# Kernel tuning notes

Hardware: AMD Instinct MI355X
Metric: run time of the kernel (lower is better)

Reference implementation:

```python
import jax, jax.numpy as jnp
import numpy as np

B, H, S, D = 2, 16, 2048, 64

def setup_inputs() -> dict:
    key = jax.random.key(0)
    kq, kk, kv = jax.random.split(key, 3)
    query = jax.random.normal(kq, (B, H, S, D), dtype=jnp.float32)
    key_t = jax.random.normal(kk, (B, H, S, D), dtype=jnp.float32)
    value = jax.random.normal(kv, (B, H, S, D), dtype=jnp.float32)
    return {"query": query, "key": key_t, "value": value}

def reference(query, key, value):
    d_k = query.shape[-1]
    scale = 1.0 / jnp.sqrt(jnp.asarray(d_k, dtype=query.dtype))
    # scores: [B, H, S, S]
    scores = jnp.einsum('bhqd,bhkd->bhqk', query, key) * scale
    p_attn = jax.nn.softmax(scores, axis=-1)
    output = jnp.einsum('bhqk,bhkd->bhqd', p_attn, value)
    return (output, p_attn)
```

## Files before the change

kernel.cpp:

```cpp
#include <hip/hip_runtime.h>

#define SS 2048
#define DD 64
#define QB 64
#define KVB 64
#define NT (SS / KVB)

typedef unsigned short ushort_t;
typedef __attribute__((ext_vector_type(4)))  float f32x4;
typedef __attribute__((ext_vector_type(16))) float f32x16;
typedef __attribute__((ext_vector_type(8)))  short bf16x8;
typedef __attribute__((ext_vector_type(2)))  unsigned int u32x2;

static __device__ __forceinline__ unsigned short f2bf(float f) {
    unsigned u = __builtin_bit_cast(unsigned, f);
    u += 0x7FFFu + ((u >> 16) & 1u);
    return (unsigned short)(u >> 16);
}

static __device__ __forceinline__ f32x16 zero16() {
    f32x16 z;
#pragma unroll
    for (int i = 0; i < 16; ++i) z[i] = 0.f;
    return z;
}

union PFrag { bf16x8 v; unsigned w[4]; };

#define GLL16(src, dst) \
    __builtin_amdgcn_global_load_lds((const __attribute__((address_space(1))) void*)(src), \
                                     (__attribute__((address_space(3))) void*)(dst), 16, 0, 0)

__global__ void cvt_bf16(const float* __restrict__ src, ushort_t* __restrict__ dst,
                         int n8, float scale)
{
    int i = blockIdx.x * blockDim.x + threadIdx.x;
    if (i >= n8) return;
    f32x4 a = ((const f32x4*)src)[2 * i];
    f32x4 b = ((const f32x4*)src)[2 * i + 1];
    bf16x8 o;
#pragma unroll
    for (int j = 0; j < 4; ++j) o[j] = (short)f2bf(a[j] * scale);
#pragma unroll
    for (int j = 0; j < 4; ++j) o[4 + j] = (short)f2bf(b[j] * scale);
    ((bf16x8*)dst)[i] = o;
}

__global__ void transposeV(const float* __restrict__ V, ushort_t* __restrict__ Vt)
{
    __shared__ float tile[64][65];
    const int tid = threadIdx.x;
    const int hh = blockIdx.x >> 5;
    const int kt = blockIdx.x & 31;

#pragma unroll
    for (int it = 0; it < 4; ++it) {
        int m = it * 256 + tid;
        int r = m >> 4, c4 = m & 15;
        f32x4 v = *(const f32x4*)(V + ((size_t)(hh * SS + kt * 64 + r)) * DD + c4 * 4);
#pragma unroll
        for (int j = 0; j < 4; ++j) tile[r][c4 * 4 + j] = v[j];
    }
    __syncthreads();
#pragma unroll
    for (int it = 0; it < 2; ++it) {
        int m = it * 256 + tid;
        int d = m >> 3, c8 = m & 7;
        bf16x8 o;
#pragma unroll
        for (int j = 0; j < 8; ++j) o[j] = (short)f2bf(tile[c8 * 8 + j][d]);
        *(bf16x8*)(Vt + ((size_t)hh * DD + d) * SS + kt * 64 + c8 * 8) = o;
    }
}

__global__ __launch_bounds__(256, 4)
void attn_main4(const float* __restrict__ gQ, const ushort_t* __restrict__ Kbf,
                const ushort_t* __restrict__ Vtbf, float* __restrict__ gO,
                float* __restrict__ gP)
{
    __shared__ float lsm[4][32];
    __shared__ __attribute__((aligned(16))) char shraw[33792];
    ushort_t* stage = (ushort_t*)shraw;
    float*    osm   = (float*)shraw;

    const int tid  = threadIdx.x;
    const int lane = tid & 63;
    const int wave = tid >> 6;
    const int lo5  = lane & 31;
    const int hi   = lane >> 5;
    const int qs   = wave >> 1;
    const int sub  = wave & 1;

    const int bid  = blockIdx.x;
    const int wg   = (bid & 7) * 128 + (bid >> 3);
    const int head = wg >> 5;
    const int q0b  = (wg & 31) * QB;

    const float*    Qh = gQ   + (size_t)head * SS * DD;
    const ushort_t* Kh = Kbf  + (size_t)head * SS * DD;
    const ushort_t* Vh = Vtbf + (size_t)head * DD * SS;
    float* Oh = gO + (size_t)head * SS * DD;
    float* Ph = gP + (size_t)head * SS * SS;

    const float SCALE = 0.125f * 1.44269504088896340736f;

    const int qrow = q0b + qs * 32 + lo5;
    bf16x8 qf[4];
#pragma unroll
    for (int ks = 0; ks < 4; ++ks) {
        const float* qp = Qh + (size_t)qrow * DD + ks * 16 + hi * 8;
        f32x4 a = *(const f32x4*)(qp);
        f32x4 b = *(const f32x4*)(qp + 4);
        bf16x8 o;
#pragma unroll
        for (int j = 0; j < 4; ++j) o[j] = (short)f2bf(a[j] * SCALE);
#pragma unroll
        for (int j = 0; j < 4; ++j) o[4 + j] = (short)f2bf(b[j] * SCALE);
        qf[ks] = o;
    }

    const int lgrp = lane >> 3;
    const int lchk = (lane & 7) ^ lgrp;
    const ushort_t* srcK[2]; const ushort_t* srcV[2];
#pragma unroll
    for (int j = 0; j < 2; ++j) {
        int W = wave * 2 + j;
        srcK[j] = Kh + (size_t)(W * 8 + lgrp) * DD + lchk * 8;
        srcV[j] = Vh + (size_t)(W * 8 + lgrp) * SS + lchk * 8;
    }
    const int kvl = sub * 32 + lo5;

#pragma unroll
    for (int j = 0; j < 2; ++j) GLL16(srcK[j], stage + (wave * 2 + j) * 512);
    __syncthreads();

    float ls0 = 0.f, ls1 = 0.f;
    for (int t = 0; t < NT; ++t) {
        const int buf = t & 1;
        if (t + 1 < NT) {
#pragma unroll
            for (int j = 0; j < 2; ++j)
                GLL16(srcK[j] + (size_t)(t + 1) * KVB * DD,
                      stage + (buf ^ 1) * 8192 + (wave * 2 + j) * 512);
        }
        const ushort_t* Ksb = stage + buf * 8192;
        f32x16 acc = zero16();
#pragma unroll
        for (int ks = 0; ks < 4; ++ks) {
            bf16x8 kf = *(const bf16x8*)(Ksb + kvl * 64 + ((((ks * 2) + hi) ^ (kvl & 7)) << 3));
            acc = __builtin_amdgcn_mfma_f32_32x32x16_bf16(kf, qf[ks], acc, 0, 0, 0);
        }
#pragma unroll
        for (int r = 0; r < 16; r += 2) {
            ls0 += __builtin_exp2f(acc[r]);
            ls1 += __builtin_exp2f(acc[r + 1]);
        }
        __syncthreads();
    }
    float lsum = ls0 + ls1;
    lsum += __shfl_xor(lsum, 32);
    lsm[wave][lo5] = lsum;
    __syncthreads();
    const float rinv = 1.0f / (lsm[qs * 2][lo5] + lsm[qs * 2 + 1][lo5]);

    f32x16 o0 = zero16(), o1 = zero16();
    float* prow_base = Ph + (size_t)qrow * SS;

#pragma unroll
    for (int j = 0; j < 2; ++j) {
        GLL16(srcK[j], stage + (wave * 2 + j) * 512);
        GLL16(srcV[j], stage + 4096 + (wave * 2 + j) * 512);
    }
    __syncthreads();

    for (int t = 0; t < NT; ++t) {
        const int buf = t & 1;
        if (t + 1 < NT) {
#pragma unroll
            for (int j = 0; j < 2; ++j) {
                GLL16(srcK[j] + (size_t)(t + 1) * KVB * DD,
                      stage + (buf ^ 1) * 8192 + (wave * 2 + j) * 512);
                GLL16(srcV[j] + (size_t)(t + 1) * KVB,
                      stage + (buf ^ 1) * 8192 + 4096 + (wave * 2 + j) * 512);
            }
        }
        const ushort_t* Ksb = stage + buf * 8192;
        const ushort_t* Vtb = Ksb + 4096;

        f32x16 acc = zero16();
#pragma unroll
        for (int ks = 0; ks < 4; ++ks) {
            bf16x8 kf = *(const bf16x8*)(Ksb + kvl * 64 + ((((ks * 2) + hi) ^ (kvl & 7)) << 3));
            acc = __builtin_amdgcn_mfma_f32_32x32x16_bf16(kf, qf[ks], acc, 0, 0, 0);
        }
        float pr[16];
#pragma unroll
        for (int r = 0; r < 16; ++r) pr[r] = __builtin_exp2f(acc[r]);

        float* prow = prow_base + t * KVB + sub * 32;
#pragma unroll
        for (int g = 0; g < 4; ++g) {
            f32x4 st = { pr[4*g+0] * rinv, pr[4*g+1] * rinv, pr[4*g+2] * rinv, pr[4*g+3] * rinv };
            *(f32x4*)(prow + g * 8 + hi * 4) = st;
        }

        unsigned u[8];
#pragma unroll
        for (int j = 0; j < 8; ++j)
            u[j] = (unsigned)f2bf(pr[2*j]) | ((unsigned)f2bf(pr[2*j+1]) << 16);

        unsigned s0 = __shfl_xor(u[0], 32), s1 = __shfl_xor(u[1], 32);
        unsigned s2 = __shfl_xor(u[2], 32), s3 = __shfl_xor(u[3], 32);
        unsigned s4 = __shfl_xor(u[4], 32), s5 = __shfl_xor(u[5], 32);
        unsigned s6 = __shfl_xor(u[6], 32), s7 = __shfl_xor(u[7], 32);
        PFrag pf0, pf1;
        pf0.w[0] = hi ? s2 : u[0];  pf0.w[1] = hi ? s3 : u[1];
        pf0.w[2] = hi ? u[2] : s0;  pf0.w[3] = hi ? u[3] : s1;
        pf1.w[0] = hi ? s6 : u[4];  pf1.w[1] = hi ? s7 : u[5];
        pf1.w[2] = hi ? u[6] : s4;  pf1.w[3] = hi ? u[7] : s5;

#pragma unroll
        for (int dt = 0; dt < 2; ++dt) {
            int drow = dt * 32 + lo5;
            int c0 = ((sub * 4) + 0 + hi) ^ (drow & 7);
            int c1 = ((sub * 4) + 2 + hi) ^ (drow & 7);
            bf16x8 vf0 = *(const bf16x8*)(Vtb + drow * 64 + (c0 << 3));
            bf16x8 vf1 = *(const bf16x8*)(Vtb + drow * 64 + (c1 << 3));
            f32x16& od = dt ? o1 : o0;
            od = __builtin_amdgcn_mfma_f32_32x32x16_bf16(vf0, pf0.v, od, 0, 0, 0);
            od = __builtin_amdgcn_mfma_f32_32x32x16_bf16(vf1, pf1.v, od, 0, 0, 0);
        }

        __syncthreads();
    }

#pragma unroll
    for (int dt = 0; dt < 2; ++dt) {
        const f32x16& od = dt ? o1 : o0;
#pragma unroll
        for (int g = 0; g < 4; ++g) {
#pragma unroll
            for (int j = 0; j < 4; ++j) {
                int d = dt * 32 + g * 8 + hi * 4 + j;
                osm[(wave * 64 + d) * 33 + lo5] = od[4 * g + j];
            }
        }
    }
    __syncthreads();
    {
        const int p  = tid >> 7;
        const int q  = (tid >> 2) & 31;
        const int d0 = (tid & 3) * 16;
        const float rq = 1.0f / (lsm[2 * p][q] + lsm[2 * p + 1][q]);
        float* op = Oh + (size_t)(q0b + p * 32 + q) * DD + d0;
#pragma unroll
        for (int v4 = 0; v4 < 4; ++v4) {
            f32x4 st;
#pragma unroll
            for (int j = 0; j < 4; ++j) {
                int d = d0 + v4 * 4 + j;
                st[j] = (osm[((2 * p) * 64 + d) * 33 + q] +
                         osm[((2 * p + 1) * 64 + d) * 33 + q]) * rq;
            }
            *(f32x4*)(op + v4 * 4) = st;
        }
    }
}

__global__ __launch_bounds__(256, 2)
void attn_fused(const float* __restrict__ gQ, const float* __restrict__ gK,
                const float* __restrict__ gV, float* __restrict__ gO,
                float* __restrict__ gP)
{
    __shared__ unsigned short Qs[128 * DD];
    __shared__ unsigned short Ks[64 * DD];
    __shared__ unsigned short Vt[DD * 64];

    const int tid  = threadIdx.x;
    const int lane = tid & 63;
    const int wave = tid >> 6;
    const int lo5  = lane & 31;
    const int hi   = lane >> 5;

    const int head = blockIdx.x >> 4;
    const int q0b  = (blockIdx.x & 15) * 128;

    const float* Qh = gQ + (size_t)head * SS * DD;
    const float* Kh = gK + (size_t)head * SS * DD;
    const float* Vh = gV + (size_t)head * SS * DD;
    float* Oh = gO + (size_t)head * SS * DD;
    float* Ph = gP + (size_t)head * SS * SS;

    const float SCALE = 0.125f * 1.44269504088896340736f;

#pragma unroll
    for (int it = 0; it < 8; ++it) {
        int m = it * 256 + tid;
        int q = m >> 4, d4 = m & 15;
        f32x4 v = *(const f32x4*)(Qh + (size_t)(q0b + q) * DD + d4 * 4);
        unsigned a = (unsigned)f2bf(v.x * SCALE) | ((unsigned)f2bf(v.y * SCALE) << 16);
        unsigned b = (unsigned)f2bf(v.z * SCALE) | ((unsigned)f2bf(v.w * SCALE) << 16);
        u32x2 w; w.x = a; w.y = b;
        *(u32x2*)(Qs + q * 64 + d4 * 4) = w;
    }
    __syncthreads();

    const int qrow = wave * 32 + lo5;
    bf16x8 qf[4];
#pragma unroll
    for (int ks = 0; ks < 4; ++ks)
        qf[ks] = *(const bf16x8*)(Qs + qrow * 64 + ks * 16 + hi * 8);

    auto stageK = [&](int kv0) {
#pragma unroll
        for (int it = 0; it < 4; ++it) {
            int m = it * 256 + tid;
            int kv = m >> 4, d4 = m & 15;
            f32x4 v = *(const f32x4*)(Kh + (size_t)(kv0 + kv) * DD + d4 * 4);
            unsigned a = (unsigned)f2bf(v.x) | ((unsigned)f2bf(v.y) << 16);
            unsigned b = (unsigned)f2bf(v.z) | ((unsigned)f2bf(v.w) << 16);
            int c16 = (d4 >> 1) ^ (kv & 7);
            u32x2 w; w.x = a; w.y = b;
            *(u32x2*)(Ks + kv * 64 + c16 * 8 + (d4 & 1) * 4) = w;
        }
    };
    auto stageV = [&](int kv0) {
#pragma unroll
        for (int it = 0; it < 2; ++it) {
            int m = it * 256 + tid;
            int kv2 = m >> 4, d4 = m & 15;
            const float* p0 = Vh + (size_t)(kv0 + kv2 * 2) * DD + d4 * 4;
            f32x4 v0 = *(const f32x4*)(p0);
            f32x4 v1 = *(const f32x4*)(p0 + DD);
#pragma unroll
            for (int c = 0; c < 4; ++c) {
                int d = d4 * 4 + c;
                unsigned u = (unsigned)f2bf(v0[c]) | ((unsigned)f2bf(v1[c]) << 16);
                int c16 = (kv2 >> 2) ^ (d & 7);
                *(unsigned*)(Vt + d * 64 + c16 * 8 + (kv2 & 3) * 2) = u;
            }
        }
    };

    float m_run = -1e30f, l_run = 0.f;
    for (int kv0 = 0; kv0 < SS; kv0 += 64) {
        __syncthreads();
        stageK(kv0);
        __syncthreads();
#pragma unroll
        for (int sub = 0; sub < 2; ++sub) {
            f32x16 acc = zero16();
            int kvl = sub * 32 + lo5;
#pragma unroll
            for (int ks = 0; ks < 4; ++ks) {
                bf16x8 kf = *(const bf16x8*)(Ks + kvl * 64 + ((((ks * 2) + hi) ^ (kvl & 7)) << 3));
                acc = __builtin_amdgcn_mfma_f32_32x32x16_bf16(kf, qf[ks], acc, 0, 0, 0);
            }
            float tm = acc[0];
#pragma unroll
            for (int r = 1; r < 16; ++r) tm = fmaxf(tm, acc[r]);
            float mn = fmaxf(m_run, tm);
            float sum = 0.f;
#pragma unroll
            for (int r = 0; r < 16; ++r) sum += __builtin_exp2f(acc[r] - mn);
            l_run = l_run * __builtin_exp2f(m_run - mn) + sum;
            m_run = mn;
        }
    }
    {
        float mo = __shfl_xor(m_run, 32);
        float mf = fmaxf(m_run, mo);
        float la = l_run * __builtin_exp2f(m_run - mf);
        float lb = __shfl_xor(la, 32);
        l_run = la + lb;
        m_run = mf;
    }
    const float rinv = 1.0f / l_run;

    f32x16 o0 = zero16(), o1 = zero16();
    const int qg = q0b + wave * 32 + lo5;
    float* prow_base = Ph + (size_t)qg * SS;

    for (int kv0 = 0; kv0 < SS; kv0 += 64) {
        __syncthreads();
        stageK(kv0);
        stageV(kv0);
        __syncthreads();
#pragma unroll
        for (int sub = 0; sub < 2; ++sub) {
            f32x16 acc = zero16();
            int kvl = sub * 32 + lo5;
#pragma unroll
            for (int ks = 0; ks < 4; ++ks) {
                bf16x8 kf = *(const bf16x8*)(Ks + kvl * 64 + ((((ks * 2) + hi) ^ (kvl & 7)) << 3));
                acc = __builtin_amdgcn_mfma_f32_32x32x16_bf16(kf, qf[ks], acc, 0, 0, 0);
            }
            float pr[16];
#pragma unroll
            for (int r = 0; r < 16; ++r) pr[r] = __builtin_exp2f(acc[r] - m_run);

            float* prow = prow_base + kv0 + sub * 32;
#pragma unroll
            for (int g = 0; g < 4; ++g) {
                f32x4 st = { pr[4*g+0] * rinv, pr[4*g+1] * rinv, pr[4*g+2] * rinv, pr[4*g+3] * rinv };
                *(f32x4*)(prow + g * 8 + hi * 4) = st;
            }

            unsigned u[8];
#pragma unroll
            for (int j = 0; j < 8; ++j)
                u[j] = (unsigned)f2bf(pr[2*j]) | ((unsigned)f2bf(pr[2*j+1]) << 16);

            unsigned s0 = __shfl_xor(u[0], 32), s1 = __shfl_xor(u[1], 32);
            unsigned s2 = __shfl_xor(u[2], 32), s3 = __shfl_xor(u[3], 32);
            unsigned s4 = __shfl_xor(u[4], 32), s5 = __shfl_xor(u[5], 32);
            unsigned s6 = __shfl_xor(u[6], 32), s7 = __shfl_xor(u[7], 32);
            PFrag pf0, pf1;
            pf0.w[0] = hi ? s2 : u[0];  pf0.w[1] = hi ? s3 : u[1];
            pf0.w[2] = hi ? u[2] : s0;  pf0.w[3] = hi ? u[3] : s1;
            pf1.w[0] = hi ? s6 : u[4];  pf1.w[1] = hi ? s7 : u[5];
            pf1.w[2] = hi ? u[6] : s4;  pf1.w[3] = hi ? u[7] : s5;

#pragma unroll
            for (int dt = 0; dt < 2; ++dt) {
                int drow = dt * 32 + lo5;
                int c0 = ((sub * 4) + 0 + hi) ^ (drow & 7);
                int c1 = ((sub * 4) + 2 + hi) ^ (drow & 7);
                bf16x8 vf0 = *(const bf16x8*)(Vt + drow * 64 + (c0 << 3));
                bf16x8 vf1 = *(const bf16x8*)(Vt + drow * 64 + (c1 << 3));
                f32x16& od = dt ? o1 : o0;
                od = __builtin_amdgcn_mfma_f32_32x32x16_bf16(vf0, pf0.v, od, 0, 0, 0);
                od = __builtin_amdgcn_mfma_f32_32x32x16_bf16(vf1, pf1.v, od, 0, 0, 0);
            }
        }
    }

    float* orow = Oh + (size_t)qg * DD;
#pragma unroll
    for (int dt = 0; dt < 2; ++dt) {
        const f32x16& od = dt ? o1 : o0;
#pragma unroll
        for (int g = 0; g < 4; ++g) {
            f32x4 st = { od[4*g+0] * rinv, od[4*g+1] * rinv, od[4*g+2] * rinv, od[4*g+3] * rinv };
            *(f32x4*)(orow + dt * 32 + g * 8 + hi * 4) = st;
        }
    }
}

extern "C" void kernel_launch(void* const* d_in, const int* in_sizes, int n_in,
                              void* d_out, int out_size, void* d_ws, size_t ws_size,
                              hipStream_t stream) {
    const float* Q = (const float*)d_in[0];
    const float* K = (const float*)d_in[1];
    const float* V = (const float*)d_in[2];
    float* O = (float*)d_out;
    float* P = O + (size_t)2 * 16 * SS * DD;

    const size_t HD = (size_t)32 * SS * DD;
    const size_t need = 2 * HD * sizeof(ushort_t);

    if (ws_size >= need) {
        ushort_t* Kbf  = (ushort_t*)d_ws;
        ushort_t* Vtbf = Kbf + HD;
        int n8 = (int)(HD / 8);
        hipLaunchKernelGGL(cvt_bf16, dim3(n8 / 256), dim3(256), 0, stream, K, Kbf, n8, 1.0f);
        hipLaunchKernelGGL(transposeV, dim3(1024), dim3(256), 0, stream, V, Vtbf);
        hipLaunchKernelGGL(attn_main4, dim3(1024), dim3(256), 0, stream, Q, Kbf, Vtbf, O, P);
    } else {
        hipLaunchKernelGGL(attn_fused, dim3(512), dim3(256), 0, stream, Q, K, V, O, P);
    }
}
```

Baseline: 212.3 us.

## Split row-sum pass into separate kernel with finer work split

Moves the softmax denominator computation out of the main attention kernel into a separate l_pass kernel. That kernel uses 32-row query blocks and splits the KV range across four waves, reading K directly from global memory with no LDS staging or barriers. The reciprocal row sums go to workspace and are read by b_pass, which now only computes P and O. This aims for more parallelism and less synchronization in the first pass, at the cost of an extra launch, a larger workspace requirement, and K being read again from global memory.

```diff
diff --git a/kernel.cpp b/kernel.cpp
--- a/kernel.cpp
+++ b/kernel.cpp
@@ -74,11 +74,78 @@
 }
 
 __global__ __launch_bounds__(256, 4)
-void attn_main4(const float* __restrict__ gQ, const ushort_t* __restrict__ Kbf,
-                const ushort_t* __restrict__ Vtbf, float* __restrict__ gO,
-                float* __restrict__ gP)
+void l_pass(const float* __restrict__ gQ, const ushort_t* __restrict__ Kbf,
+            float* __restrict__ wsR)
 {
     __shared__ float lsm[4][32];
+
+    const int tid  = threadIdx.x;
+    const int lane = tid & 63;
+    const int wave = tid >> 6;
+    const int lo5  = lane & 31;
+    const int hi   = lane >> 5;
+
+    const int bid  = blockIdx.x;
+    const int wg   = (bid & 7) * 256 + (bid >> 3);
+    const int head = wg >> 6;
+    const int q0b  = (wg & 63) * 32;
+
+    const float*    Qh = gQ  + (size_t)head * SS * DD;
+    const ushort_t* Kh = Kbf + (size_t)head * SS * DD;
+
+    const float SCALE = 0.125f * 1.44269504088896340736f;
+
+    const int qrow = q0b + lo5;
+    bf16x8 qf[4];
+#pragma unroll
+    for (int ks = 0; ks < 4; ++ks) {
+        const float* qp = Qh + (size_t)qrow * DD + ks * 16 + hi * 8;
+        f32x4 a = *(const f32x4*)(qp);
+        f32x4 b = *(const f32x4*)(qp + 4);
+        bf16x8 o;
+#pragma unroll
+        for (int j = 0; j < 4; ++j) o[j] = (short)f2bf(a[j] * SCALE);
+#pragma unroll
+        for (int j = 0; j < 4; ++j) o[4 + j] = (short)f2bf(b[j] * SCALE);
+        qf[ks] = o;
+    }
+
+    const int kv_base = wave * 512;
+    float ls0 = 0.f, ls1 = 0.f;
+#pragma unroll 2
+    for (int t = 0; t < 8; ++t) {
+        int kv0 = kv_base + t * 64;
+#pragma unroll
+        for (int sub = 0; sub < 2; ++sub) {
+            f32x16 acc = zero16();
+            const ushort_t* kp = Kh + (size_t)(kv0 + sub * 32 + lo5) * DD + hi * 8;
+#pragma unroll
+            for (int ks = 0; ks < 4; ++ks) {
+                bf16x8 kf = *(const bf16x8*)(kp + ks * 16);
+                acc = __builtin_amdgcn_mfma_f32_32x32x16_bf16(kf, qf[ks], acc, 0, 0, 0);
+            }
+#pragma unroll
+            for (int r = 0; r < 16; r += 2) {
+                ls0 += __builtin_exp2f(acc[r]);
+                ls1 += __builtin_exp2f(acc[r + 1]);
+            }
+        }
+    }
+    float lsum = ls0 + ls1;
+    lsum += __shfl_xor(lsum, 32);
+    lsm[wave][lo5] = lsum;
+    __syncthreads();
+    if (tid < 32) {
+        float l = lsm[0][tid] + lsm[1][tid] + lsm[2][tid] + lsm[3][tid];
+        wsR[(size_t)head * SS + q0b + tid] = 1.0f / l;
+    }
+}
+
+__global__ __launch_bounds__(256, 4)
+void b_pass(const float* __restrict__ gQ, const ushort_t* __restrict__ Kbf,
+            const ushort_t* __restrict__ Vtbf, const float* __restrict__ wsR,
+            float* __restrict__ gO, float* __restrict__ gP)
+{
     __shared__ __attribute__((aligned(16))) char shraw[33792];
     ushort_t* stage = (ushort_t*)shraw;
     float*    osm   = (float*)shraw;
@@ -118,6 +185,7 @@
         for (int j = 0; j < 4; ++j) o[4 + j] = (short)f2bf(b[j] * SCALE);
         qf[ks] = o;
     }
+    const float rinv = wsR[(size_t)head * SS + qrow];
 
     const int lgrp = lane >> 3;
     const int lchk = (lane & 7) ^ lgrp;
@@ -129,39 +197,6 @@
         srcV[j] = Vh + (size_t)(W * 8 + lgrp) * SS + lchk * 8;
     }
     const int kvl = sub * 32 + lo5;
-
-#pragma unroll
-    for (int j = 0; j < 2; ++j) GLL16(srcK[j], stage + (wave * 2 + j) * 512);
-    __syncthreads();
-
-    float ls0 = 0.f, ls1 = 0.f;
-    for (int t = 0; t < NT; ++t) {
-        const int buf = t & 1;
-        if (t + 1 < NT) {
-#pragma unroll
-            for (int j = 0; j < 2; ++j)
-                GLL16(srcK[j] + (size_t)(t + 1) * KVB * DD,
-                      stage + (buf ^ 1) * 8192 + (wave * 2 + j) * 512);
-        }
-        const ushort_t* Ksb = stage + buf * 8192;
-        f32x16 acc = zero16();
-#pragma unroll
-        for (int ks = 0; ks < 4; ++ks) {
-            bf16x8 kf = *(const bf16x8*)(Ksb + kvl * 64 + ((((ks * 2) + hi) ^ (kvl & 7)) << 3));
-            acc = __builtin_amdgcn_mfma_f32_32x32x16_bf16(kf, qf[ks], acc, 0, 0, 0);
-        }
-#pragma unroll
-        for (int r = 0; r < 16; r += 2) {
-            ls0 += __builtin_exp2f(acc[r]);
-            ls1 += __builtin_exp2f(acc[r + 1]);
-        }
-        __syncthreads();
-    }
-    float lsum = ls0 + ls1;
-    lsum += __shfl_xor(lsum, 32);
-    lsm[wave][lo5] = lsum;
-    __syncthreads();
-    const float rinv = 1.0f / (lsm[qs * 2][lo5] + lsm[qs * 2 + 1][lo5]);
 
     f32x16 o0 = zero16(), o1 = zero16();
     float* prow_base = Ph + (size_t)qrow * SS;
@@ -251,7 +286,7 @@
         const int p  = tid >> 7;
         const int q  = (tid >> 2) & 31;
         const int d0 = (tid & 3) * 16;
-        const float rq = 1.0f / (lsm[2 * p][q] + lsm[2 * p + 1][q]);
+        const float rq = wsR[(size_t)head * SS + q0b + p * 32 + q];
         float* op = Oh + (size_t)(q0b + p * 32 + q) * DD + d0;
 #pragma unroll
         for (int v4 = 0; v4 < 4; ++v4) {
@@ -457,15 +492,18 @@
     float* P = O + (size_t)2 * 16 * SS * DD;
 
     const size_t HD = (size_t)32 * SS * DD;
-    const size_t need = 2 * HD * sizeof(ushort_t);
+    const size_t RN = (size_t)32 * SS;
+    const size_t need = 2 * HD * sizeof(ushort_t) + RN * sizeof(float);
 
     if (ws_size >= need) {
         ushort_t* Kbf  = (ushort_t*)d_ws;
         ushort_t* Vtbf = Kbf + HD;
+        float*    wsR  = (float*)(Vtbf + HD);
         int n8 = (int)(HD / 8);
         hipLaunchKernelGGL(cvt_bf16, dim3(n8 / 256), dim3(256), 0, stream, K, Kbf, n8, 1.0f);
         hipLaunchKernelGGL(transposeV, dim3(1024), dim3(256), 0, stream, V, Vtbf);
-        hipLaunchKernelGGL(attn_main4, dim3(1024), dim3(256), 0, stream, Q, Kbf, Vtbf, O, P);
+        hipLaunchKernelGGL(l_pass, dim3(2048), dim3(256), 0, stream, Q, Kbf, wsR);
+        hipLaunchKernelGGL(b_pass, dim3(1024), dim3(256), 0, stream, Q, Kbf, Vtbf, wsR, O, P);
     } else {
         hipLaunchKernelGGL(attn_fused, dim3(512), dim3(256), 0, stream, Q, K, V, O, P);
     }
```

Result: slower. 256.3 us (+20.7%).

## Split row-sum pass across waves and use per-wave private K/V staging

Applied to the files above, without the earlier changes.

In the first pass (softmax denominators), each wave now reads its own quarter of the keys straight from global memory for both 32-row query halves. The per-wave sums are then combined through shared memory, which removes the per-tile block barriers from that pass. In the second pass, each wave double-buffers its own K/V slice in a private 16 KB LDS region, waits with explicit vmcnt counts, and skips the per-iteration __syncthreads. The cost is twice the LDS (64 KB) and a cut in occupancy from 4 to 2 blocks. It also adds redundant K loads across waves and hand-tuned waitcnt logic that could break if the compiler reorders loads.

```diff
diff --git a/kernel.cpp b/kernel.cpp
--- a/kernel.cpp
+++ b/kernel.cpp
@@ -73,13 +73,13 @@
     }
 }
 
-__global__ __launch_bounds__(256, 4)
-void attn_main4(const float* __restrict__ gQ, const ushort_t* __restrict__ Kbf,
+__global__ __launch_bounds__(256, 2)
+void attn_main7(const float* __restrict__ gQ, const ushort_t* __restrict__ Kbf,
                 const ushort_t* __restrict__ Vtbf, float* __restrict__ gO,
                 float* __restrict__ gP)
 {
-    __shared__ float lsm[4][32];
-    __shared__ __attribute__((aligned(16))) char shraw[33792];
+    __shared__ float lsm[4][2][32];
+    __shared__ __attribute__((aligned(16))) char shraw[65536];
     ushort_t* stage = (ushort_t*)shraw;
     float*    osm   = (float*)shraw;
 
@@ -104,94 +104,105 @@
 
     const float SCALE = 0.125f * 1.44269504088896340736f;
 
+    bf16x8 qf2[2][4];
+#pragma unroll
+    for (int p = 0; p < 2; ++p)
+#pragma unroll
+        for (int ks = 0; ks < 4; ++ks) {
+            const float* qp = Qh + (size_t)(q0b + p * 32 + lo5) * DD + ks * 16 + hi * 8;
+            f32x4 a = *(const f32x4*)(qp);
+            f32x4 b = *(const f32x4*)(qp + 4);
+            bf16x8 o;
+#pragma unroll
+            for (int j = 0; j < 4; ++j) o[j] = (short)f2bf(a[j] * SCALE);
+#pragma unroll
+            for (int j = 0; j < 4; ++j) o[4 + j] = (short)f2bf(b[j] * SCALE);
+            qf2[p][ks] = o;
+        }
+
+    float la00 = 0.f, la01 = 0.f, la10 = 0.f, la11 = 0.f;
+#pragma unroll 2
+    for (int t = 0; t < 8; ++t) {
+        int kv0 = wave * 512 + t * 64;
+#pragma unroll
+        for (int s = 0; s < 2; ++s) {
+            const ushort_t* kp = Kh + (size_t)(kv0 + s * 32 + lo5) * DD + hi * 8;
+            bf16x8 kf[4];
+#pragma unroll
+            for (int ks = 0; ks < 4; ++ks) kf[ks] = *(const bf16x8*)(kp + ks * 16);
+            f32x16 a0 = zero16(), a1 = zero16();
+#pragma unroll
+            for (int ks = 0; ks < 4; ++ks) {
+                a0 = __builtin_amdgcn_mfma_f32_32x32x16_bf16(kf[ks], qf2[0][ks], a0, 0, 0, 0);
+                a1 = __builtin_amdgcn_mfma_f32_32x32x16_bf16(kf[ks], qf2[1][ks], a1, 0, 0, 0);
+            }
+#pragma unroll
+            for (int r = 0; r < 16; r += 2) {
+                la00 += __builtin_exp2f(a0[r]);
+                la01 += __builtin_exp2f(a0[r + 1]);
+                la10 += __builtin_exp2f(a1[r]);
+                la11 += __builtin_exp2f(a1[r + 1]);
+            }
+        }
+    }
+    {
+        float l0 = la00 + la01, l1 = la10 + la11;
+        l0 += __shfl_xor(l0, 32);
+        l1 += __shfl_xor(l1, 32);
+        lsm[wave][0][lo5] = l0;
+        lsm[wave][1][lo5] = l1;
+    }
+    __syncthreads();
+    const float rinv = 1.0f / (lsm[0][qs][lo5] + lsm[1][qs][lo5] +
+                               lsm[2][qs][lo5] + lsm[3][qs][lo5]);
+
+    ushort_t* wbase = stage + wave * 8192;
+
+    const int l8g = lane >> 3, l8c = lane & 7;
+    const int kchk = l8c ^ l8g;
+    const int l4g = lane >> 2, l4c = lane & 3;
+    const int vchk = l4c ^ (l4g & 3);
+    const ushort_t* sK[4];
+    const ushort_t* sV[4];
+#pragma unroll
+    for (int j = 0; j < 4; ++j) {
+        sK[j] = Kh + (size_t)(sub * 32 + j * 8 + l8g) * DD + kchk * 8;
+        sV[j] = Vh + (size_t)(j * 16 + l4g) * SS + sub * 32 + vchk * 8;
+    }
+
+    auto STAGE_B = [&](int tt, int b) {
+        ushort_t* kb = wbase + b * 4096;
+#pragma unroll
+        for (int j = 0; j < 4; ++j)
+            GLL16(sK[j] + (size_t)tt * KVB * DD, kb + j * 512);
+#pragma unroll
+        for (int j = 0; j < 4; ++j)
+            GLL16(sV[j] + tt * KVB, kb + 2048 + j * 512);
+    };
+
+    f32x16 o0 = zero16(), o1 = zero16();
     const int qrow = q0b + qs * 32 + lo5;
-    bf16x8 qf[4];
-#pragma unroll
-    for (int ks = 0; ks < 4; ++ks) {
-        const float* qp = Qh + (size_t)qrow * DD + ks * 16 + hi * 8;
-        f32x4 a = *(const f32x4*)(qp);
-        f32x4 b = *(const f32x4*)(qp + 4);
-        bf16x8 o;
-#pragma unroll
-        for (int j = 0; j < 4; ++j) o[j] = (short)f2bf(a[j] * SCALE);
-#pragma unroll
-        for (int j = 0; j < 4; ++j) o[4 + j] = (short)f2bf(b[j] * SCALE);
-        qf[ks] = o;
-    }
-
-    const int lgrp = lane >> 3;
-    const int lchk = (lane & 7) ^ lgrp;
-    const ushort_t* srcK[2]; const ushort_t* srcV[2];
-#pragma unroll
-    for (int j = 0; j < 2; ++j) {
-        int W = wave * 2 + j;
-        srcK[j] = Kh + (size_t)(W * 8 + lgrp) * DD + lchk * 8;
-        srcV[j] = Vh + (size_t)(W * 8 + lgrp) * SS + lchk * 8;
-    }
-    const int kvl = sub * 32 + lo5;
-
-#pragma unroll
-    for (int j = 0; j < 2; ++j) GLL16(srcK[j], stage + (wave * 2 + j) * 512);
-    __syncthreads();
-
-    float ls0 = 0.f, ls1 = 0.f;
+    float* prow_base = Ph + (size_t)qrow * SS;
+
+    STAGE_B(0, 0);
+
     for (int t = 0; t < NT; ++t) {
-        const int buf = t & 1;
-        if (t + 1 < NT) {
-#pragma unroll
-            for (int j = 0; j < 2; ++j)
-                GLL16(srcK[j] + (size_t)(t + 1) * KVB * DD,
-                      stage + (buf ^ 1) * 8192 + (wave * 2 + j) * 512);
-        }
-        const ushort_t* Ksb = stage + buf * 8192;
+        const int b = t & 1;
+        if (t + 1 < NT) STAGE_B(t + 1, b ^ 1);
+        __builtin_amdgcn_sched_barrier(0);
+        if (t == 0)            asm volatile("s_waitcnt vmcnt(8)"  ::: "memory");
+        else if (t + 1 < NT)   asm volatile("s_waitcnt vmcnt(12)" ::: "memory");
+        else                   asm volatile("s_waitcnt vmcnt(4)"  ::: "memory");
+        __builtin_amdgcn_sched_barrier(0);
+
+        const ushort_t* Ksb = wbase + b * 4096;
+        const ushort_t* Vtb = Ksb + 2048;
+
         f32x16 acc = zero16();
 #pragma unroll
         for (int ks = 0; ks < 4; ++ks) {
-            bf16x8 kf = *(const bf16x8*)(Ksb + kvl * 64 + ((((ks * 2) + hi) ^ (kvl & 7)) << 3));
-            acc = __builtin_amdgcn_mfma_f32_32x32x16_bf16(kf, qf[ks], acc, 0, 0, 0);
-        }
-#pragma unroll
-        for (int r = 0; r < 16; r += 2) {
-            ls0 += __builtin_exp2f(acc[r]);
-            ls1 += __builtin_exp2f(acc[r + 1]);
-        }
-        __syncthreads();
-    }
-    float lsum = ls0 + ls1;
-    lsum += __shfl_xor(lsum, 32);
-    lsm[wave][lo5] = lsum;
-    __syncthreads();
-    const float rinv = 1.0f / (lsm[qs * 2][lo5] + lsm[qs * 2 + 1][lo5]);
-
-    f32x16 o0 = zero16(), o1 = zero16();
-    float* prow_base = Ph + (size_t)qrow * SS;
-
-#pragma unroll
-    for (int j = 0; j < 2; ++j) {
-        GLL16(srcK[j], stage + (wave * 2 + j) * 512);
-        GLL16(srcV[j], stage + 4096 + (wave * 2 + j) * 512);
-    }
-    __syncthreads();
-
-    for (int t = 0; t < NT; ++t) {
-        const int buf = t & 1;
-        if (t + 1 < NT) {
-#pragma unroll
-            for (int j = 0; j < 2; ++j) {
-                GLL16(srcK[j] + (size_t)(t + 1) * KVB * DD,
-                      stage + (buf ^ 1) * 8192 + (wave * 2 + j) * 512);
-                GLL16(srcV[j] + (size_t)(t + 1) * KVB,
-                      stage + (buf ^ 1) * 8192 + 4096 + (wave * 2 + j) * 512);
-            }
-        }
-        const ushort_t* Ksb = stage + buf * 8192;
-        const ushort_t* Vtb = Ksb + 4096;
-
-        f32x16 acc = zero16();
-#pragma unroll
-        for (int ks = 0; ks < 4; ++ks) {
-            bf16x8 kf = *(const bf16x8*)(Ksb + kvl * 64 + ((((ks * 2) + hi) ^ (kvl & 7)) << 3));
-            acc = __builtin_amdgcn_mfma_f32_32x32x16_bf16(kf, qf[ks], acc, 0, 0, 0);
+            bf16x8 kf = *(const bf16x8*)(Ksb + lo5 * 64 + ((((ks * 2) + hi) ^ (lo5 & 7)) << 3));
+            acc = __builtin_amdgcn_mfma_f32_32x32x16_bf16(kf, qf2[qs][ks], acc, 0, 0, 0);
         }
         float pr[16];
 #pragma unroll
@@ -203,12 +214,12 @@
             f32x4 st = { pr[4*g+0] * rinv, pr[4*g+1] * rinv, pr[4*g+2] * rinv, pr[4*g+3] * rinv };
             *(f32x4*)(prow + g * 8 + hi * 4) = st;
         }
+        __builtin_amdgcn_sched_barrier(0);
 
         unsigned u[8];
 #pragma unroll
         for (int j = 0; j < 8; ++j)
             u[j] = (unsigned)f2bf(pr[2*j]) | ((unsigned)f2bf(pr[2*j+1]) << 16);
-
         unsigned s0 = __shfl_xor(u[0], 32), s1 = __shfl_xor(u[1], 32);
         unsigned s2 = __shfl_xor(u[2], 32), s3 = __shfl_xor(u[3], 32);
         unsigned s4 = __shfl_xor(u[4], 32), s5 = __shfl_xor(u[5], 32);
@@ -222,18 +233,17 @@
 #pragma unroll
         for (int dt = 0; dt < 2; ++dt) {
             int drow = dt * 32 + lo5;
-            int c0 = ((sub * 4) + 0 + hi) ^ (drow & 7);
-            int c1 = ((sub * 4) + 2 + hi) ^ (drow & 7);
-            bf16x8 vf0 = *(const bf16x8*)(Vtb + drow * 64 + (c0 << 3));
-            bf16x8 vf1 = *(const bf16x8*)(Vtb + drow * 64 + (c1 << 3));
+            int c0 = (0 + hi) ^ (drow & 3);
+            int c1 = (2 + hi) ^ (drow & 3);
+            bf16x8 vf0 = *(const bf16x8*)(Vtb + drow * 32 + (c0 << 3));
+            bf16x8 vf1 = *(const bf16x8*)(Vtb + drow * 32 + (c1 << 3));
             f32x16& od = dt ? o1 : o0;
             od = __builtin_amdgcn_mfma_f32_32x32x16_bf16(vf0, pf0.v, od, 0, 0, 0);
             od = __builtin_amdgcn_mfma_f32_32x32x16_bf16(vf1, pf1.v, od, 0, 0, 0);
         }
-
-        __syncthreads();
-    }
-
+    }
+
+    __syncthreads();
 #pragma unroll
     for (int dt = 0; dt < 2; ++dt) {
         const f32x16& od = dt ? o1 : o0;
@@ -251,7 +261,7 @@
         const int p  = tid >> 7;
         const int q  = (tid >> 2) & 31;
         const int d0 = (tid & 3) * 16;
-        const float rq = 1.0f / (lsm[2 * p][q] + lsm[2 * p + 1][q]);
+        const float rq = 1.0f / (lsm[0][p][q] + lsm[1][p][q] + lsm[2][p][q] + lsm[3][p][q]);
         float* op = Oh + (size_t)(q0b + p * 32 + q) * DD + d0;
 #pragma unroll
         for (int v4 = 0; v4 < 4; ++v4) {
@@ -465,7 +475,7 @@
         int n8 = (int)(HD / 8);
         hipLaunchKernelGGL(cvt_bf16, dim3(n8 / 256), dim3(256), 0, stream, K, Kbf, n8, 1.0f);
         hipLaunchKernelGGL(transposeV, dim3(1024), dim3(256), 0, stream, V, Vtbf);
-        hipLaunchKernelGGL(attn_main4, dim3(1024), dim3(256), 0, stream, Q, Kbf, Vtbf, O, P);
+        hipLaunchKernelGGL(attn_main7, dim3(1024), dim3(256), 0, stream, Q, Kbf, Vtbf, O, P);
     } else {
         hipLaunchKernelGGL(attn_fused, dim3(512), dim3(256), 0, stream, Q, K, V, O, P);
     }
```

Result: slower. 250.2 us (+17.9%).

## Double KV tile to 128 per barrier and merge K/V prep kernels

Applied to the files above, without the earlier changes.

Raises the KV tile from 64 to 128 rows, so each pipeline step stages twice as much K and V^T in LDS and processes two 64-wide sub-blocks between barriers. This halves the number of __syncthreads and loop iterations per pass. It also fuses the K conversion and V transpose into one prep launch to save a kernel launch. In exchange LDS use doubles to 64KB and launch bounds drop to 2 blocks per CU, which lowers occupancy.

```diff
diff --git a/kernel.cpp b/kernel.cpp
--- a/kernel.cpp
+++ b/kernel.cpp
@@ -3,7 +3,7 @@
 #define SS 2048
 #define DD 64
 #define QB 64
-#define KVB 64
+#define KVB 128
 #define NT (SS / KVB)
 
 typedef unsigned short ushort_t;
@@ -31,28 +31,26 @@
     __builtin_amdgcn_global_load_lds((const __attribute__((address_space(1))) void*)(src), \
                                      (__attribute__((address_space(3))) void*)(dst), 16, 0, 0)
 
-__global__ void cvt_bf16(const float* __restrict__ src, ushort_t* __restrict__ dst,
-                         int n8, float scale)
+__global__ void prep(const float* __restrict__ K, const float* __restrict__ V,
+                     ushort_t* __restrict__ Kbf, ushort_t* __restrict__ Vt)
 {
-    int i = blockIdx.x * blockDim.x + threadIdx.x;
-    if (i >= n8) return;
-    f32x4 a = ((const f32x4*)src)[2 * i];
-    f32x4 b = ((const f32x4*)src)[2 * i + 1];
-    bf16x8 o;
-#pragma unroll
-    for (int j = 0; j < 4; ++j) o[j] = (short)f2bf(a[j] * scale);
-#pragma unroll
-    for (int j = 0; j < 4; ++j) o[4 + j] = (short)f2bf(b[j] * scale);
-    ((bf16x8*)dst)[i] = o;
-}
-
-__global__ void transposeV(const float* __restrict__ V, ushort_t* __restrict__ Vt)
-{
+    const int tid = threadIdx.x;
+    if (blockIdx.x < 2048) {
+        int i = blockIdx.x * 256 + tid;
+        f32x4 a = ((const f32x4*)K)[2 * i];
+        f32x4 b = ((const f32x4*)K)[2 * i + 1];
+        bf16x8 o;
+#pragma unroll
+        for (int j = 0; j < 4; ++j) o[j] = (short)f2bf(a[j]);
+#pragma unroll
+        for (int j = 0; j < 4; ++j) o[4 + j] = (short)f2bf(b[j]);
+        ((bf16x8*)Kbf)[i] = o;
+        return;
+    }
     __shared__ float tile[64][65];
-    const int tid = threadIdx.x;
-    const int hh = blockIdx.x >> 5;
-    const int kt = blockIdx.x & 31;
-
+    const int bid2 = blockIdx.x - 2048;
+    const int hh = bid2 >> 5;
+    const int kt = bid2 & 31;
 #pragma unroll
     for (int it = 0; it < 4; ++it) {
         int m = it * 256 + tid;
@@ -73,13 +71,13 @@
     }
 }
 
-__global__ __launch_bounds__(256, 4)
-void attn_main4(const float* __restrict__ gQ, const ushort_t* __restrict__ Kbf,
+__global__ __launch_bounds__(256, 2)
+void attn_main9(const float* __restrict__ gQ, const ushort_t* __restrict__ Kbf,
                 const ushort_t* __restrict__ Vtbf, float* __restrict__ gO,
                 float* __restrict__ gP)
 {
     __shared__ float lsm[4][32];
-    __shared__ __attribute__((aligned(16))) char shraw[33792];
+    __shared__ __attribute__((aligned(16))) char shraw[65536];
     ushort_t* stage = (ushort_t*)shraw;
     float*    osm   = (float*)shraw;
 
@@ -120,18 +118,20 @@
     }
 
     const int lgrp = lane >> 3;
-    const int lchk = (lane & 7) ^ lgrp;
-    const ushort_t* srcK[2]; const ushort_t* srcV[2];
-#pragma unroll
-    for (int j = 0; j < 2; ++j) {
-        int W = wave * 2 + j;
-        srcK[j] = Kh + (size_t)(W * 8 + lgrp) * DD + lchk * 8;
-        srcV[j] = Vh + (size_t)(W * 8 + lgrp) * SS + lchk * 8;
-    }
-    const int kvl = sub * 32 + lo5;
-
-#pragma unroll
-    for (int j = 0; j < 2; ++j) GLL16(srcK[j], stage + (wave * 2 + j) * 512);
+    const int kchk = (lane & 7) ^ lgrp;
+    const ushort_t* srcK[4];
+    const ushort_t* srcV[4];
+#pragma unroll
+    for (int j = 0; j < 4; ++j) {
+        int W = wave * 4 + j;
+        srcK[j] = Kh + (size_t)(W * 8 + lgrp) * DD + kchk * 8;
+        int d = W * 4 + (lane >> 4);
+        int vchk = (lane & 15) ^ (d & 7);
+        srcV[j] = Vh + (size_t)d * SS + vchk * 8;
+    }
+
+#pragma unroll
+    for (int j = 0; j < 4; ++j) GLL16(srcK[j], stage + (wave * 4 + j) * 512);
     __syncthreads();
 
     float ls0 = 0.f, ls1 = 0.f;
@@ -139,21 +139,25 @@
         const int buf = t & 1;
         if (t + 1 < NT) {
 #pragma unroll
-            for (int j = 0; j < 2; ++j)
+            for (int j = 0; j < 4; ++j)
                 GLL16(srcK[j] + (size_t)(t + 1) * KVB * DD,
-                      stage + (buf ^ 1) * 8192 + (wave * 2 + j) * 512);
-        }
-        const ushort_t* Ksb = stage + buf * 8192;
-        f32x16 acc = zero16();
-#pragma unroll
-        for (int ks = 0; ks < 4; ++ks) {
-            bf16x8 kf = *(const bf16x8*)(Ksb + kvl * 64 + ((((ks * 2) + hi) ^ (kvl & 7)) << 3));
-            acc = __builtin_amdgcn_mfma_f32_32x32x16_bf16(kf, qf[ks], acc, 0, 0, 0);
-        }
-#pragma unroll
-        for (int r = 0; r < 16; r += 2) {
-            ls0 += __builtin_exp2f(acc[r]);
-            ls1 += __builtin_exp2f(acc[r + 1]);
+                      stage + (buf ^ 1) * 16384 + (wave * 4 + j) * 512);
+        }
+        const ushort_t* Ksb = stage + buf * 16384;
+#pragma unroll
+        for (int g64 = 0; g64 < 2; ++g64) {
+            const int kvl = g64 * 64 + sub * 32 + lo5;
+            f32x16 acc = zero16();
+#pragma unroll
+            for (int ks = 0; ks < 4; ++ks) {
+                bf16x8 kf = *(const bf16x8*)(Ksb + kvl * 64 + ((((ks * 2) + hi) ^ (kvl & 7)) << 3));
+                acc = __builtin_amdgcn_mfma_f32_32x32x16_bf16(kf, qf[ks], acc, 0, 0, 0);
+            }
+#pragma unroll
+            for (int r = 0; r < 16; r += 2) {
+                ls0 += __builtin_exp2f(acc[r]);
+                ls1 += __builtin_exp2f(acc[r + 1]);
+            }
         }
         __syncthreads();
     }
@@ -167,9 +171,9 @@
     float* prow_base = Ph + (size_t)qrow * SS;
 
 #pragma unroll
-    for (int j = 0; j < 2; ++j) {
-        GLL16(srcK[j], stage + (wave * 2 + j) * 512);
-        GLL16(srcV[j], stage + 4096 + (wave * 2 + j) * 512);
+    for (int j = 0; j < 4; ++j) {
+        GLL16(srcK[j], stage + (wave * 4 + j) * 512);
+        GLL16(srcV[j], stage + 8192 + (wave * 4 + j) * 512);
     }
     __syncthreads();
 
@@ -177,60 +181,62 @@
         const int buf = t & 1;
         if (t + 1 < NT) {
 #pragma unroll
-            for (int j = 0; j < 2; ++j) {
+            for (int j = 0; j < 4; ++j) {
                 GLL16(srcK[j] + (size_t)(t + 1) * KVB * DD,
-                      stage + (buf ^ 1) * 8192 + (wave * 2 + j) * 512);
+                      stage + (buf ^ 1) * 16384 + (wave * 4 + j) * 512);
                 GLL16(srcV[j] + (size_t)(t + 1) * KVB,
-                      stage + (buf ^ 1) * 8192 + 4096 + (wave * 2 + j) * 512);
-            }
-        }
-        const ushort_t* Ksb = stage + buf * 8192;
-        const ushort_t* Vtb = Ksb + 4096;
-
-        f32x16 acc = zero16();
-#pragma unroll
-        for (int ks = 0; ks < 4; ++ks) {
-            bf16x8 kf = *(const bf16x8*)(Ksb + kvl * 64 + ((((ks * 2) + hi) ^ (kvl & 7)) << 3));
-            acc = __builtin_amdgcn_mfma_f32_32x32x16_bf16(kf, qf[ks], acc, 0, 0, 0);
-        }
-        float pr[16];
-#pragma unroll
-        for (int r = 0; r < 16; ++r) pr[r] = __builtin_exp2f(acc[r]);
-
-        float* prow = prow_base + t * KVB + sub * 32;
-#pragma unroll
-        for (int g = 0; g < 4; ++g) {
-            f32x4 st = { pr[4*g+0] * rinv, pr[4*g+1] * rinv, pr[4*g+2] * rinv, pr[4*g+3] * rinv };
-            *(f32x4*)(prow + g * 8 + hi * 4) = st;
-        }
-
-        unsigned u[8];
-#pragma unroll
-        for (int j = 0; j < 8; ++j)
-            u[j] = (unsigned)f2bf(pr[2*j]) | ((unsigned)f2bf(pr[2*j+1]) << 16);
-
-        unsigned s0 = __shfl_xor(u[0], 32), s1 = __shfl_xor(u[1], 32);
-        unsigned s2 = __shfl_xor(u[2], 32), s3 = __shfl_xor(u[3], 32);
-        unsigned s4 = __shfl_xor(u[4], 32), s5 = __shfl_xor(u[5], 32);
-        unsigned s6 = __shfl_xor(u[6], 32), s7 = __shfl_xor(u[7], 32);
-        PFrag pf0, pf1;
-        pf0.w[0] = hi ? s2 : u[0];  pf0.w[1] = hi ? s3 : u[1];
-        pf0.w[2] = hi ? u[2] : s0;  pf0.w[3] = hi ? u[3] : s1;
-        pf1.w[0] = hi ? s6 : u[4];  pf1.w[1] = hi ? s7 : u[5];
-        pf1.w[2] = hi ? u[6] : s4;  pf1.w[3] = hi ? u[7] : s5;
-
-#pragma unroll
-        for (int dt = 0; dt < 2; ++dt) {
-            int drow = dt * 32 + lo5;
-            int c0 = ((sub * 4) + 0 + hi) ^ (drow & 7);
-            int c1 = ((sub * 4) + 2 + hi) ^ (drow & 7);
-            bf16x8 vf0 = *(const bf16x8*)(Vtb + drow * 64 + (c0 << 3));
-            bf16x8 vf1 = *(const bf16x8*)(Vtb + drow * 64 + (c1 << 3));
-            f32x16& od = dt ? o1 : o0;
-            od = __builtin_amdgcn_mfma_f32_32x32x16_bf16(vf0, pf0.v, od, 0, 0, 0);
-            od = __builtin_amdgcn_mfma_f32_32x32x16_bf16(vf1, pf1.v, od, 0, 0, 0);
-        }
-
+                      stage + (buf ^ 1) * 16384 + 8192 + (wave * 4 + j) * 512);
+            }
+        }
+        const ushort_t* Ksb = stage + buf * 16384;
+        const ushort_t* Vtb = Ksb + 8192;
+
+#pragma unroll
+        for (int g64 = 0; g64 < 2; ++g64) {
+            const int kvl = g64 * 64 + sub * 32 + lo5;
+            f32x16 acc = zero16();
+#pragma unroll
+            for (int ks = 0; ks < 4; ++ks) {
+                bf16x8 kf = *(const bf16x8*)(Ksb + kvl * 64 + ((((ks * 2) + hi) ^ (kvl & 7)) << 3));
+                acc = __builtin_amdgcn_mfma_f32_32x32x16_bf16(kf, qf[ks], acc, 0, 0, 0);
+            }
+            float pr[16];
+#pragma unroll
+            for (int r = 0; r < 16; ++r) pr[r] = __builtin_exp2f(acc[r]);
+
+            float* prow = prow_base + t * KVB + g64 * 64 + sub * 32;
+#pragma unroll
+            for (int g = 0; g < 4; ++g) {
+                f32x4 st = { pr[4*g+0] * rinv, pr[4*g+1] * rinv, pr[4*g+2] * rinv, pr[4*g+3] * rinv };
+                *(f32x4*)(prow + g * 8 + hi * 4) = st;
+            }
+
+            unsigned u[8];
+#pragma unroll
+            for (int j = 0; j < 8; ++j)
+                u[j] = (unsigned)f2bf(pr[2*j]) | ((unsigned)f2bf(pr[2*j+1]) << 16);
+            unsigned s0 = __shfl_xor(u[0], 32), s1 = __shfl_xor(u[1], 32);
+            unsigned s2 = __shfl_xor(u[2], 32), s3 = __shfl_xor(u[3], 32);
+            unsigned s4 = __shfl_xor(u[4], 32), s5 = __shfl_xor(u[5], 32);
+            unsigned s6 = __shfl_xor(u[6], 32), s7 = __shfl_xor(u[7], 32);
+            PFrag pf0, pf1;
+            pf0.w[0] = hi ? s2 : u[0];  pf0.w[1] = hi ? s3 : u[1];
+            pf0.w[2] = hi ? u[2] : s0;  pf0.w[3] = hi ? u[3] : s1;
+            pf1.w[0] = hi ? s6 : u[4];  pf1.w[1] = hi ? s7 : u[5];
+            pf1.w[2] = hi ? u[6] : s4;  pf1.w[3] = hi ? u[7] : s5;
+
+#pragma unroll
+            for (int dt = 0; dt < 2; ++dt) {
+                int drow = dt * 32 + lo5;
+                int c0 = (g64 << 3) + (((sub * 4) + 0 + hi) ^ (drow & 7));
+                int c1 = (g64 << 3) + (((sub * 4) + 2 + hi) ^ (drow & 7));
+                bf16x8 vf0 = *(const bf16x8*)(Vtb + drow * 128 + (c0 << 3));
+                bf16x8 vf1 = *(const bf16x8*)(Vtb + drow * 128 + (c1 << 3));
+                f32x16& od = dt ? o1 : o0;
+                od = __builtin_amdgcn_mfma_f32_32x32x16_bf16(vf0, pf0.v, od, 0, 0, 0);
+                od = __builtin_amdgcn_mfma_f32_32x32x16_bf16(vf1, pf1.v, od, 0, 0, 0);
+            }
+        }
         __syncthreads();
     }
 
@@ -462,10 +468,8 @@
     if (ws_size >= need) {
         ushort_t* Kbf  = (ushort_t*)d_ws;
         ushort_t* Vtbf = Kbf + HD;
-        int n8 = (int)(HD / 8);
-        hipLaunchKernelGGL(cvt_bf16, dim3(n8 / 256), dim3(256), 0, stream, K, Kbf, n8, 1.0f);
-        hipLaunchKernelGGL(transposeV, dim3(1024), dim3(256), 0, stream, V, Vtbf);
-        hipLaunchKernelGGL(attn_main4, dim3(1024), dim3(256), 0, stream, Q, Kbf, Vtbf, O, P);
+        hipLaunchKernelGGL(prep, dim3(3072), dim3(256), 0, stream, K, V, Kbf, Vtbf);
+        hipLaunchKernelGGL(attn_main9, dim3(1024), dim3(256), 0, stream, Q, Kbf, Vtbf, O, P);
     } else {
         hipLaunchKernelGGL(attn_fused, dim3(512), dim3(256), 0, stream, Q, K, V, O, P);
     }
```

Result: slower. 216.9 us (+2.2%).
